# Performance work log

Measured on AMD Instinct MI355X. Metric: run time of the kernel, lower is better.

Reference implementation:

```python
import jax, jax.numpy as jnp
import numpy as np

N = 100000        # nodes
E = 3200000       # random edges (avg degree 32); self-loops added in reference
IN, HID, HEADS, OUT = 10, 32, 2, 4
NEG_SLOPE = 0.2   # PyG GATConv default leaky_relu slope


def setup_inputs() -> dict:
    key = jax.random.key(0)
    ks = jax.random.split(key, 16)
    s = 0.1
    return {
        "x": jax.random.normal(ks[0], (N, IN), jnp.float32),
        "edge_index": jax.random.randint(ks[1], (2, E), 0, N),
        "W1": jax.random.normal(ks[2], (IN, HEADS * HID), jnp.float32) * s,
        "a1s": jax.random.normal(ks[3], (HEADS, HID), jnp.float32) * s,
        "a1d": jax.random.normal(ks[4], (HEADS, HID), jnp.float32) * s,
        "b1": jnp.zeros((HEADS * HID,), jnp.float32),
        "W2": jax.random.normal(ks[5], (HEADS * HID, HEADS * HID), jnp.float32) * s,
        "a2s": jax.random.normal(ks[6], (HEADS, HID), jnp.float32) * s,
        "a2d": jax.random.normal(ks[7], (HEADS, HID), jnp.float32) * s,
        "b2": jnp.zeros((HEADS * HID,), jnp.float32),
        "W3": jax.random.normal(ks[8], (HEADS * HID, OUT), jnp.float32) * s,
        "a3s": jax.random.normal(ks[9], (1, OUT), jnp.float32) * s,
        "a3d": jax.random.normal(ks[10], (1, OUT), jnp.float32) * s,
        "b3": jnp.zeros((OUT,), jnp.float32),
    }


def gat_layer(x, src, dst, W, a_src, a_dst, b, concat):
    """One PyG-style GATConv (shared src/dst linear, self-loops already in src/dst)."""
    heads, oc = a_src.shape
    h = (x @ W).reshape(-1, heads, oc)                    # [N, H, C]
    asc = jnp.einsum('nhc,hc->nh', h, a_src)              # [N, H]
    adc = jnp.einsum('nhc,hc->nh', h, a_dst)              # [N, H]
    e = jax.nn.leaky_relu(asc[src] + adc[dst], NEG_SLOPE) # [Etot, H]
    m = jax.ops.segment_max(e, dst, num_segments=N)       # segment softmax over dst
    ex = jnp.exp(e - m[dst])
    z = jax.ops.segment_sum(ex, dst, num_segments=N)
    alpha = ex / z[dst]                                   # [Etot, H]
    out = jax.ops.segment_sum(h[src] * alpha[:, :, None], dst, num_segments=N)
    out = out.reshape(-1, heads * oc) if concat else out.mean(axis=1)
    return out + b


def reference(x, edge_index, W1, a1s, a1d, b1, W2, a2s, a2d, b2, W3, a3s, a3d, b3):
    loops = jnp.arange(N)
    src = jnp.concatenate([edge_index[0], loops])
    dst = jnp.concatenate([edge_index[1], loops])
    h = jax.nn.relu(gat_layer(x, src, dst, W1, a1s, a1d, b1, True))
    h = jax.nn.relu(gat_layer(h, src, dst, W2, a2s, a2d, b2, True))
    h = gat_layer(h, src, dst, W3, a3s, a3d, b3, False)
    return jax.nn.sigmoid(h) * 100.0
```

## Files before the change

kernel.cpp:

```cpp
#include <hip/hip_runtime.h>
#include <hip/hip_bf16.h>
#include <math.h>

#define NEG_SLOPE 0.2f
#define PSHIFT 8
#define PSIZE 256
#define NPARTS_MAX 392
#define B1 768
#define CELL_CAP 32
#define PCAP 10240
#define LCSR_CAP 10240
#define CHUNK 64

typedef int vint2 __attribute__((ext_vector_type(2)));
typedef int vint4 __attribute__((ext_vector_type(4)));
typedef short bf16x8 __attribute__((ext_vector_type(8)));
typedef float floatx4 __attribute__((ext_vector_type(4)));

__device__ __forceinline__ float lrelu(float v) { return fmaxf(v, NEG_SLOPE * v); }

__device__ __forceinline__ unsigned short f2bf(float f) {
    unsigned int b = __float_as_uint(f);
    b += 0x7fffu + ((b >> 16) & 1u);
    return (unsigned short)(b >> 16);
}
__device__ __forceinline__ float bf2f(unsigned short u) {
    return __uint_as_float((unsigned int)u << 16);
}

__global__ void k_part(const int* __restrict__ src, const int* __restrict__ dst, int E,
                       int* __restrict__ pairs, int* __restrict__ ptot, int nparts) {
    __shared__ int stage[NPARTS_MAX * CELL_CAP];
    __shared__ int lcnt[NPARTS_MAX];
    int tid = threadIdx.x, blk = blockIdx.x;
    for (int i = tid; i < nparts; i += 256) lcnt[i] = 0;
    __syncthreads();
    int per = ((E + B1 * 4 - 1) / (B1 * 4)) * 4;
    int s = blk * per, e = min(E, s + per);
    bool al = ((E & 3) == 0);
    for (int i0 = s + tid * 4; i0 < e; i0 += 1024) {
        int dv[4], sv[4], nv;
        if (al && i0 + 4 <= e) {
            vint4 d4 = __builtin_nontemporal_load((const vint4*)(dst + i0));
            vint4 s4 = __builtin_nontemporal_load((const vint4*)(src + i0));
            dv[0] = d4.x; dv[1] = d4.y; dv[2] = d4.z; dv[3] = d4.w;
            sv[0] = s4.x; sv[1] = s4.y; sv[2] = s4.z; sv[3] = s4.w;
            nv = 4;
        } else {
            nv = min(4, e - i0);
            for (int k = 0; k < nv; ++k) {
                dv[k] = __builtin_nontemporal_load(dst + i0 + k);
                sv[k] = __builtin_nontemporal_load(src + i0 + k);
            }
        }
        for (int k = 0; k < nv; ++k) {
            int p = dv[k] >> PSHIFT;
            int pos = atomicAdd(&lcnt[p], 1);
            if (pos < CELL_CAP)
                stage[p * CELL_CAP + pos] = (sv[k] << PSHIFT) | (dv[k] & (PSIZE - 1));
        }
    }
    __syncthreads();
    for (int p = tid; p < nparts; p += 256) {
        int tgt = min(lcnt[p], CELL_CAP);
        if (tgt == 0) continue;
        int base = atomicAdd(&ptot[p], tgt);
        if (base + tgt > PCAP) tgt = max(0, PCAP - base);
        int* gp = pairs + (size_t)p * PCAP + base;
        const int* sp = &stage[p * CELL_CAP];
        for (int j = 0; j < tgt; ++j) gp[j] = sp[j];
    }
}

__global__ void k_pscan(const int* __restrict__ ptot, int* __restrict__ pbase,
                        int* __restrict__ row, int nparts, int N) {
    __shared__ int sh[512];
    int tid = threadIdx.x;
    int v = (tid < nparts) ? min(ptot[tid], PCAP) : 0;
    sh[tid] = v;
    __syncthreads();
    for (int off = 1; off < 512; off <<= 1) {
        int t = (tid >= off) ? sh[tid - off] : 0;
        __syncthreads();
        sh[tid] += t;
        __syncthreads();
    }
    if (tid < nparts) pbase[tid] = sh[tid] - v;
    if (tid == nparts - 1) row[N] = sh[tid];
}

__global__ void k_scat2(const int* __restrict__ pairs, const int* __restrict__ ptot,
                        const int* __restrict__ pbase, int* __restrict__ row,
                        int* __restrict__ csr, int N) {
    __shared__ int lcsr[LCSR_CAP];
    __shared__ int lhist[PSIZE], lcur[PSIZE];
    int part = blockIdx.x;
    int lo = part << PSHIFT;
    int npart = min(PSIZE, N - lo);
    int tid = threadIdx.x;
    int cnt = min(ptot[part], PCAP);
    const int* seg = pairs + (size_t)part * PCAP;
    for (int i = tid; i < PSIZE; i += 1024) lhist[i] = 0;
    __syncthreads();
    for (int i = tid; i < cnt; i += 1024)
        atomicAdd(&lhist[__builtin_nontemporal_load(&seg[i]) & (PSIZE - 1)], 1);
    __syncthreads();
    if (tid < PSIZE) lcur[tid] = lhist[tid];
    __syncthreads();
    for (int off = 1; off < PSIZE; off <<= 1) {
        int t = 0;
        if (tid < PSIZE && tid >= off) t = lcur[tid - off];
        __syncthreads();
        if (tid < PSIZE) lcur[tid] += t;
        __syncthreads();
    }
    int pb = pbase[part];
    if (tid < npart) row[lo + tid] = pb + lcur[tid] - lhist[tid];
    if (tid < PSIZE) lcur[tid] -= lhist[tid];
    __syncthreads();
    for (int i = tid; i < cnt; i += 1024) {
        int v = __builtin_nontemporal_load(&seg[i]);
        int pos = atomicAdd(&lcur[v & (PSIZE - 1)], 1);
        if (pos < LCSR_CAP) lcsr[pos] = (unsigned)v >> PSHIFT;
    }
    __syncthreads();
    for (int i = tid; i < cnt; i += 1024)
        csr[pb + i] = lcsr[i];
}

__global__ void k_lin1(const float* __restrict__ x, const float* __restrict__ W,
                       const float* __restrict__ as_, const float* __restrict__ ad_,
                       unsigned short* __restrict__ hb, float* __restrict__ asc,
                       float* __restrict__ adc, int N) {
    __shared__ float sW[10 * 64];
    int tid = threadIdx.x;
    for (int i = tid; i < 640; i += 256) sW[i] = W[i];
    __syncthreads();
    int wid = tid >> 6, lane = tid & 63;
    int n = blockIdx.x * 4 + wid;
    if (n >= N) return;
    float acc = 0.f;
#pragma unroll
    for (int k = 0; k < 10; ++k) acc += x[n * 10 + k] * sW[k * 64 + lane];
    hb[(size_t)n * 64 + lane] = f2bf(acc);
    int head = lane >> 5, cc = lane & 31;
    float rs = acc * as_[lane];
    float rd = acc * ad_[lane];
#pragma unroll
    for (int m = 16; m >= 1; m >>= 1) {
        rs += __shfl_xor(rs, m, 64);
        rd += __shfl_xor(rd, m, 64);
    }
    if (cc == 0) { asc[n * 2 + head] = rs; adc[n * 2 + head] = rd; }
}

__global__ void k_lin2(const float* __restrict__ yin, const float* __restrict__ W,
                       const float* __restrict__ as_, const float* __restrict__ ad_,
                       unsigned short* __restrict__ hb, float* __restrict__ asc,
                       float* __restrict__ adc, int N) {
    __shared__ unsigned short sW[64 * 64];
    int tid = threadIdx.x;
    for (int i = tid; i < 4096; i += 256) sW[i] = f2bf(W[i]);
    __syncthreads();
    int wid = tid >> 6, lane = tid & 63;
    int quad = lane >> 4, col = lane & 15;
    bf16x8 bfr[4][2];
#pragma unroll
    for (int blk = 0; blk < 4; ++blk)
#pragma unroll
        for (int kh = 0; kh < 2; ++kh)
#pragma unroll
            for (int j = 0; j < 8; ++j)
                bfr[blk][kh][j] = (short)sW[(kh * 32 + quad * 8 + j) * 64 + blk * 16 + col];
    float asv[4], adv[4];
#pragma unroll
    for (int blk = 0; blk < 4; ++blk) {
        asv[blk] = as_[blk * 16 + col];
        adv[blk] = ad_[blk * 16 + col];
    }
    int tile = blockIdx.x * 4 + wid;
    int nb = tile * 16;
    if (nb >= N) return;
    int mrow = nb + col; if (mrow >= N) mrow = N - 1;
    const float* yr = yin + (size_t)mrow * 64;
    bf16x8 afr[2];
#pragma unroll
    for (int kh = 0; kh < 2; ++kh) {
        const float4* p = (const float4*)(yr + kh * 32 + quad * 8);
        float4 u0 = p[0], u1 = p[1];
        afr[kh][0] = (short)f2bf(u0.x); afr[kh][1] = (short)f2bf(u0.y);
        afr[kh][2] = (short)f2bf(u0.z); afr[kh][3] = (short)f2bf(u0.w);
        afr[kh][4] = (short)f2bf(u1.x); afr[kh][5] = (short)f2bf(u1.y);
        afr[kh][6] = (short)f2bf(u1.z); afr[kh][7] = (short)f2bf(u1.w);
    }
    floatx4 acc[4];
#pragma unroll
    for (int blk = 0; blk < 4; ++blk) {
        acc[blk][0] = 0.f; acc[blk][1] = 0.f; acc[blk][2] = 0.f; acc[blk][3] = 0.f;
        acc[blk] = __builtin_amdgcn_mfma_f32_16x16x32_bf16(afr[0], bfr[blk][0], acc[blk], 0, 0, 0);
        acc[blk] = __builtin_amdgcn_mfma_f32_16x16x32_bf16(afr[1], bfr[blk][1], acc[blk], 0, 0, 0);
    }
#pragma unroll
    for (int r = 0; r < 4; ++r) {
        int m = nb + quad * 4 + r;
        if (m < N) {
#pragma unroll
            for (int blk = 0; blk < 4; ++blk)
                hb[(size_t)m * 64 + blk * 16 + col] = f2bf(acc[blk][r]);
        }
    }
    float s0[4], s1[4], d0[4], d1[4];
#pragma unroll
    for (int r = 0; r < 4; ++r) {
        s0[r] = acc[0][r] * asv[0] + acc[1][r] * asv[1];
        s1[r] = acc[2][r] * asv[2] + acc[3][r] * asv[3];
        d0[r] = acc[0][r] * adv[0] + acc[1][r] * adv[1];
        d1[r] = acc[2][r] * adv[2] + acc[3][r] * adv[3];
    }
#pragma unroll
    for (int mask = 8; mask >= 1; mask >>= 1) {
#pragma unroll
        for (int r = 0; r < 4; ++r) {
            s0[r] += __shfl_xor(s0[r], mask, 64);
            s1[r] += __shfl_xor(s1[r], mask, 64);
            d0[r] += __shfl_xor(d0[r], mask, 64);
            d1[r] += __shfl_xor(d1[r], mask, 64);
        }
    }
    if (col < 4) {
        int m = nb + quad * 4 + col;
        if (m < N) {
            float vs0 = col == 0 ? s0[0] : col == 1 ? s0[1] : col == 2 ? s0[2] : s0[3];
            float vs1 = col == 0 ? s1[0] : col == 1 ? s1[1] : col == 2 ? s1[2] : s1[3];
            float vd0 = col == 0 ? d0[0] : col == 1 ? d0[1] : col == 2 ? d0[2] : d0[3];
            float vd1 = col == 0 ? d1[0] : col == 1 ? d1[1] : col == 2 ? d1[2] : d1[3];
            asc[m * 2 + 0] = vs0; asc[m * 2 + 1] = vs1;
            adc[m * 2 + 0] = vd0; adc[m * 2 + 1] = vd1;
        }
    }
}

__global__ void k_agg(const unsigned short* __restrict__ hb, const float* __restrict__ asc,
                      const float* __restrict__ adc, const int* __restrict__ row,
                      const int* __restrict__ csr_src, const float* __restrict__ bias,
                      float* __restrict__ yout, int N, int do_relu) {
    __shared__ vint2 tbl[4][2 * CHUNK];
    int tid = threadIdx.x;
    int wid = tid >> 6, lane = tid & 63;
    int n = blockIdx.x * 4 + wid;
    if (n >= N) return;
    int s = row[n], e = row[n + 1];
    int head = lane >> 5, sub = lane & 31;
    int cho = lane & 7;
    int hq = (lane >> 2) & 1;
    int jo = lane >> 3;
    int cho16 = cho << 4;
    float2 ad = ((const float2*)adc)[n];
    float adch = head ? ad.y : ad.x;
    float2 asf = ((const float2*)asc)[n];
    float p_self_h = __expf(lrelu((head ? asf.y : asf.x) + adch));
    float zl = (sub == 0) ? p_self_h : 0.f;
    float a0 = 0.f, a1 = 0.f, a2 = 0.f, a3 = 0.f;
    float a4 = 0.f, a5 = 0.f, a6 = 0.f, a7 = 0.f;
    const char* hbB = (const char*)hb;
    vint2* mytbl = tbl[wid];
    int tb = hq << 6;
    int wbase = head << 6;
    for (int base = s; base < e; base += CHUNK) {
        int cnt = e - base; if (cnt > CHUNK) cnt = CHUNK;
#pragma unroll
        for (int h2 = 0; h2 < 2; ++h2) {
            int idx = base + sub + h2 * 32;
            int srcv = 0;
            float p_l = 0.f;
            if (idx < e) {
                srcv = csr_src[idx];
                p_l = __expf(lrelu(asc[(size_t)srcv * 2 + head] + adch));
            }
            zl += p_l;
            vint2 ent; ent.x = srcv << 7; ent.y = __float_as_int(p_l);
            mytbl[wbase | (sub + h2 * 32)] = ent;
        }
        __builtin_amdgcn_wave_barrier();
#pragma unroll 4
        for (int j = jo; j < cnt; j += 8) {
            vint2 t = mytbl[tb | j];
            vint4 pk = *(const vint4*)(hbB + (unsigned)(t.x | cho16));
            float p = __int_as_float(t.y);
            unsigned int w0 = (unsigned int)pk.x, w1 = (unsigned int)pk.y;
            unsigned int w2 = (unsigned int)pk.z, w3 = (unsigned int)pk.w;
            a0 += p * __uint_as_float(w0 << 16);
            a1 += p * __uint_as_float(w0 & 0xffff0000u);
            a2 += p * __uint_as_float(w1 << 16);
            a3 += p * __uint_as_float(w1 & 0xffff0000u);
            a4 += p * __uint_as_float(w2 << 16);
            a5 += p * __uint_as_float(w2 & 0xffff0000u);
            a6 += p * __uint_as_float(w3 << 16);
            a7 += p * __uint_as_float(w3 & 0xffff0000u);
        }
        __builtin_amdgcn_wave_barrier();
    }
#pragma unroll
    for (int msk = 8; msk <= 32; msk <<= 1) {
        a0 += __shfl_xor(a0, msk, 64); a1 += __shfl_xor(a1, msk, 64);
        a2 += __shfl_xor(a2, msk, 64); a3 += __shfl_xor(a3, msk, 64);
        a4 += __shfl_xor(a4, msk, 64); a5 += __shfl_xor(a5, msk, 64);
        a6 += __shfl_xor(a6, msk, 64); a7 += __shfl_xor(a7, msk, 64);
    }
#pragma unroll
    for (int msk = 16; msk >= 1; msk >>= 1) zl += __shfl_xor(zl, msk, 64);
    float zo = __shfl_xor(zl, 32, 64);
    float zneed = (hq == head) ? zl : zo;
    float adcm = hq ? ad.y : ad.x;
    float p_self_my = __expf(lrelu((hq ? asf.y : asf.x) + adcm));
    vint4 pks = *(const vint4*)(hbB + (((unsigned)n << 7) | (unsigned)cho16));
    {
        unsigned int w0 = (unsigned int)pks.x, w1 = (unsigned int)pks.y;
        unsigned int w2 = (unsigned int)pks.z, w3 = (unsigned int)pks.w;
        a0 += p_self_my * __uint_as_float(w0 << 16);
        a1 += p_self_my * __uint_as_float(w0 & 0xffff0000u);
        a2 += p_self_my * __uint_as_float(w1 << 16);
        a3 += p_self_my * __uint_as_float(w1 & 0xffff0000u);
        a4 += p_self_my * __uint_as_float(w2 << 16);
        a5 += p_self_my * __uint_as_float(w2 & 0xffff0000u);
        a6 += p_self_my * __uint_as_float(w3 << 16);
        a7 += p_self_my * __uint_as_float(w3 & 0xffff0000u);
    }
    float inv = 1.f / zneed;
    float4 bv0 = ((const float4*)bias)[cho * 2];
    float4 bv1 = ((const float4*)bias)[cho * 2 + 1];
    float y0 = a0 * inv + bv0.x;
    float y1 = a1 * inv + bv0.y;
    float y2 = a2 * inv + bv0.z;
    float y3 = a3 * inv + bv0.w;
    float y4 = a4 * inv + bv1.x;
    float y5 = a5 * inv + bv1.y;
    float y6 = a6 * inv + bv1.z;
    float y7 = a7 * inv + bv1.w;
    if (do_relu) {
        y0 = fmaxf(y0, 0.f); y1 = fmaxf(y1, 0.f);
        y2 = fmaxf(y2, 0.f); y3 = fmaxf(y3, 0.f);
        y4 = fmaxf(y4, 0.f); y5 = fmaxf(y5, 0.f);
        y6 = fmaxf(y6, 0.f); y7 = fmaxf(y7, 0.f);
    }
    if (jo == 0) {
        float4 o0; o0.x = y0; o0.y = y1; o0.z = y2; o0.w = y3;
        float4 o1; o1.x = y4; o1.y = y5; o1.z = y6; o1.w = y7;
        ((float4*)yout)[(size_t)n * 16 + cho * 2] = o0;
        ((float4*)yout)[(size_t)n * 16 + cho * 2 + 1] = o1;
    }
}

__global__ void k_lin3(const float* __restrict__ yin, const float* __restrict__ W3,
                       const float* __restrict__ a3s, const float* __restrict__ a3d,
                       float4* __restrict__ rec, int N) {
    __shared__ float sW[256];
    int tid = threadIdx.x;
    sW[tid] = W3[tid];
    __syncthreads();
    int t = blockIdx.x * 256 + tid;
    int n = t >> 2, c = t & 3;
    if (n >= N) return;
    float acc = 0.f;
#pragma unroll
    for (int k = 0; k < 64; ++k) acc += yin[(size_t)n * 64 + k] * sW[k * 4 + c];
    float rs = acc * a3s[c], rd = acc * a3d[c];
    rs += __shfl_xor(rs, 1, 64); rs += __shfl_xor(rs, 2, 64);
    rd += __shfl_xor(rd, 1, 64); rd += __shfl_xor(rd, 2, 64);
    float a_1 = __shfl_xor(acc, 1, 64);
    float a_2 = __shfl_xor(acc, 2, 64);
    float a_3 = __shfl_xor(acc, 3, 64);
    if (c == 0) {
        unsigned int lo = (unsigned int)f2bf(acc) | ((unsigned int)f2bf(a_1) << 16);
        unsigned int hi = (unsigned int)f2bf(a_2) | ((unsigned int)f2bf(a_3) << 16);
        float4 r;
        r.x = __uint_as_float(lo); r.y = __uint_as_float(hi);
        r.z = rs; r.w = rd;
        rec[n] = r;
    }
}

__global__ void k_agg3(const float4* __restrict__ rec, const int* __restrict__ row,
                       const int* __restrict__ csr_src, const float* __restrict__ b3,
                       float* __restrict__ out, int N) {
    int tid = threadIdx.x;
    int half = tid >> 5, lane = tid & 31;
    int n = blockIdx.x * 8 + half;
    if (n >= N) return;
    int s = row[n], e = row[n + 1];
    float4 rn = rec[n];
    float adcn = rn.w;
    float n0 = 0.f, n1 = 0.f, n2 = 0.f, n3 = 0.f, den = 0.f;
    if (lane == 0) {
        float p = __expf(lrelu(rn.z + adcn));
        unsigned int lo = __float_as_uint(rn.x), hi = __float_as_uint(rn.y);
        n0 = p * __uint_as_float(lo << 16);
        n1 = p * __uint_as_float(lo & 0xffff0000u);
        n2 = p * __uint_as_float(hi << 16);
        n3 = p * __uint_as_float(hi & 0xffff0000u);
        den = p;
    }
    for (int idx = s + lane; idx < e; idx += 32) {
        int src = csr_src[idx];
        float4 r = rec[src];
        float p = __expf(lrelu(r.z + adcn));
        unsigned int lo = __float_as_uint(r.x), hi = __float_as_uint(r.y);
        n0 += p * __uint_as_float(lo << 16);
        n1 += p * __uint_as_float(lo & 0xffff0000u);
        n2 += p * __uint_as_float(hi << 16);
        n3 += p * __uint_as_float(hi & 0xffff0000u);
        den += p;
    }
#pragma unroll
    for (int msk = 16; msk >= 1; msk >>= 1) {
        n0 += __shfl_xor(n0, msk, 64);
        n1 += __shfl_xor(n1, msk, 64);
        n2 += __shfl_xor(n2, msk, 64);
        n3 += __shfl_xor(n3, msk, 64);
        den += __shfl_xor(den, msk, 64);
    }
    if (lane < 4) {
        float num = lane == 0 ? n0 : lane == 1 ? n1 : lane == 2 ? n2 : n3;
        float v = num / den + b3[lane];
        out[n * 4 + lane] = 100.f / (1.f + __expf(-v));
    }
}

extern "C" void kernel_launch(void* const* d_in, const int* in_sizes, int n_in,
                              void* d_out, int out_size, void* d_ws, size_t ws_size,
                              hipStream_t stream) {
    const float* x   = (const float*)d_in[0];
    const int*   ei  = (const int*)d_in[1];
    const float* W1  = (const float*)d_in[2];
    const float* a1s = (const float*)d_in[3];
    const float* a1d = (const float*)d_in[4];
    const float* b1  = (const float*)d_in[5];
    const float* W2  = (const float*)d_in[6];
    const float* a2s = (const float*)d_in[7];
    const float* a2d = (const float*)d_in[8];
    const float* b2  = (const float*)d_in[9];
    const float* W3  = (const float*)d_in[10];
    const float* a3s = (const float*)d_in[11];
    const float* a3d = (const float*)d_in[12];
    const float* b3  = (const float*)d_in[13];
    float* out = (float*)d_out;

    const int N = in_sizes[0] / 10;
    const int E = in_sizes[1] / 2;
    const int* esrc = ei;
    const int* edst = ei + E;
    const int nparts = (N + PSIZE - 1) >> PSHIFT;

    char* ws = (char*)d_ws;
    size_t off = 0;
    auto alloc = [&](size_t bytes) {
        void* p = ws + off;
        off = (off + bytes + 255) & ~(size_t)255;
        return p;
    };
    int*   row   = (int*)alloc((size_t)(N + 1) * sizeof(int));
    int*   ptot  = (int*)alloc(NPARTS_MAX * sizeof(int));
    int*   pbase = (int*)alloc(NPARTS_MAX * sizeof(int));
    int*   csr   = (int*)alloc((size_t)E * sizeof(int));
    unsigned short* hb = (unsigned short*)alloc((size_t)N * 64 * sizeof(unsigned short));
    float* y     = (float*)alloc((size_t)N * 64 * sizeof(float));
    float4* rec  = (float4*)alloc((size_t)N * sizeof(float4));
    float* asc   = (float*)alloc((size_t)N * 2 * sizeof(float));
    float* adc   = (float*)alloc((size_t)N * 2 * sizeof(float));
    int* pairs = (int*)hb;

    (void)hipMemsetAsync(ptot, 0, NPARTS_MAX * sizeof(int), stream);

    const int nw = (N + 3) / 4;
    const int tiles = (N + 15) / 16;

    k_part<<<B1, 256, 0, stream>>>(esrc, edst, E, pairs, ptot, nparts);
    k_pscan<<<1, 512, 0, stream>>>(ptot, pbase, row, nparts, N);
    k_scat2<<<nparts, 1024, 0, stream>>>(pairs, ptot, pbase, row, csr, N);

    k_lin1<<<nw, 256, 0, stream>>>(x, W1, a1s, a1d, hb, asc, adc, N);
    k_agg<<<nw, 256, 0, stream>>>(hb, asc, adc, row, csr, b1, y, N, 1);
    k_lin2<<<(tiles + 3) / 4, 256, 0, stream>>>(y, W2, a2s, a2d, hb, asc, adc, N);
    k_agg<<<nw, 256, 0, stream>>>(hb, asc, adc, row, csr, b2, y, N, 1);
    k_lin3<<<(N * 4 + 255) / 256, 256, 0, stream>>>(y, W3, a3s, a3d, rec, N);
    k_agg3<<<(N + 7) / 8, 256, 0, stream>>>(rec, row, csr, b3, out, N);
}
```

Baseline: 355.4 us.

## Replace LDS edge table with wave shuffles and add nontemporal streaming accesses

The aggregation kernel no longer stages each 64-edge chunk's source offsets and attention weights in LDS. Each lane now loads one edge, computes the weights for both heads from a single float2 read of asc, and the inner loop broadcasts values with shuffles, removing the LDS table and wave barriers. The layer-3 projection is restructured so each lane reads 16 contiguous floats as vectors and computes partial dots for all four outputs before a shuffle reduction. Nontemporal loads and stores are added for streamed arrays such as csr_src, yin, yout and out. The cost is three shuffles per edge iteration in place of one LDS read, and a risk that nontemporal hints hurt if the data would have been reused from cache.

```diff
diff --git a/kernel.cpp b/kernel.cpp
--- a/kernel.cpp
+++ b/kernel.cpp
@@ -10,7 +10,6 @@
 #define CELL_CAP 32
 #define PCAP 10240
 #define LCSR_CAP 10240
-#define CHUNK 64
 
 typedef int vint2 __attribute__((ext_vector_type(2)));
 typedef int vint4 __attribute__((ext_vector_type(4)));
@@ -186,12 +185,13 @@
     bf16x8 afr[2];
 #pragma unroll
     for (int kh = 0; kh < 2; ++kh) {
-        const float4* p = (const float4*)(yr + kh * 32 + quad * 8);
-        float4 u0 = p[0], u1 = p[1];
-        afr[kh][0] = (short)f2bf(u0.x); afr[kh][1] = (short)f2bf(u0.y);
-        afr[kh][2] = (short)f2bf(u0.z); afr[kh][3] = (short)f2bf(u0.w);
-        afr[kh][4] = (short)f2bf(u1.x); afr[kh][5] = (short)f2bf(u1.y);
-        afr[kh][6] = (short)f2bf(u1.z); afr[kh][7] = (short)f2bf(u1.w);
+        const floatx4* p = (const floatx4*)(yr + kh * 32 + quad * 8);
+        floatx4 u0 = __builtin_nontemporal_load(p);
+        floatx4 u1 = __builtin_nontemporal_load(p + 1);
+        afr[kh][0] = (short)f2bf(u0[0]); afr[kh][1] = (short)f2bf(u0[1]);
+        afr[kh][2] = (short)f2bf(u0[2]); afr[kh][3] = (short)f2bf(u0[3]);
+        afr[kh][4] = (short)f2bf(u1[0]); afr[kh][5] = (short)f2bf(u1[1]);
+        afr[kh][6] = (short)f2bf(u1[2]); afr[kh][7] = (short)f2bf(u1[3]);
     }
     floatx4 acc[4];
 #pragma unroll
@@ -244,49 +244,39 @@
                       const float* __restrict__ adc, const int* __restrict__ row,
                       const int* __restrict__ csr_src, const float* __restrict__ bias,
                       float* __restrict__ yout, int N, int do_relu) {
-    __shared__ vint2 tbl[4][2 * CHUNK];
     int tid = threadIdx.x;
     int wid = tid >> 6, lane = tid & 63;
     int n = blockIdx.x * 4 + wid;
     if (n >= N) return;
     int s = row[n], e = row[n + 1];
-    int head = lane >> 5, sub = lane & 31;
     int cho = lane & 7;
     int hq = (lane >> 2) & 1;
     int jo = lane >> 3;
     int cho16 = cho << 4;
     float2 ad = ((const float2*)adc)[n];
-    float adch = head ? ad.y : ad.x;
     float2 asf = ((const float2*)asc)[n];
-    float p_self_h = __expf(lrelu((head ? asf.y : asf.x) + adch));
-    float zl = (sub == 0) ? p_self_h : 0.f;
     float a0 = 0.f, a1 = 0.f, a2 = 0.f, a3 = 0.f;
     float a4 = 0.f, a5 = 0.f, a6 = 0.f, a7 = 0.f;
+    float z0 = 0.f, z1 = 0.f;
     const char* hbB = (const char*)hb;
-    vint2* mytbl = tbl[wid];
-    int tb = hq << 6;
-    int wbase = head << 6;
-    for (int base = s; base < e; base += CHUNK) {
-        int cnt = e - base; if (cnt > CHUNK) cnt = CHUNK;
-#pragma unroll
-        for (int h2 = 0; h2 < 2; ++h2) {
-            int idx = base + sub + h2 * 32;
-            int srcv = 0;
-            float p_l = 0.f;
-            if (idx < e) {
-                srcv = csr_src[idx];
-                p_l = __expf(lrelu(asc[(size_t)srcv * 2 + head] + adch));
-            }
-            zl += p_l;
-            vint2 ent; ent.x = srcv << 7; ent.y = __float_as_int(p_l);
-            mytbl[wbase | (sub + h2 * 32)] = ent;
-        }
-        __builtin_amdgcn_wave_barrier();
+    for (int base = s; base < e; base += 64) {
+        int cnt = e - base; if (cnt > 64) cnt = 64;
+        int sv7 = 0; float p0 = 0.f, p1 = 0.f;
+        if (lane < cnt) {
+            int srcv = __builtin_nontemporal_load(csr_src + base + lane);
+            float2 av = ((const float2*)asc)[srcv];
+            p0 = __expf(lrelu(av.x + ad.x));
+            p1 = __expf(lrelu(av.y + ad.y));
+            sv7 = srcv << 7;
+        }
+        z0 += p0; z1 += p1;
 #pragma unroll 4
         for (int j = jo; j < cnt; j += 8) {
-            vint2 t = mytbl[tb | j];
-            vint4 pk = *(const vint4*)(hbB + (unsigned)(t.x | cho16));
-            float p = __int_as_float(t.y);
+            int a = __shfl(sv7, j, 64);
+            float q0 = __shfl(p0, j, 64);
+            float q1 = __shfl(p1, j, 64);
+            float p = hq ? q1 : q0;
+            vint4 pk = *(const vint4*)(hbB + (unsigned)(a | cho16));
             unsigned int w0 = (unsigned int)pk.x, w1 = (unsigned int)pk.y;
             unsigned int w2 = (unsigned int)pk.z, w3 = (unsigned int)pk.w;
             a0 += p * __uint_as_float(w0 << 16);
@@ -298,7 +288,6 @@
             a6 += p * __uint_as_float(w3 << 16);
             a7 += p * __uint_as_float(w3 & 0xffff0000u);
         }
-        __builtin_amdgcn_wave_barrier();
     }
 #pragma unroll
     for (int msk = 8; msk <= 32; msk <<= 1) {
@@ -308,11 +297,15 @@
         a6 += __shfl_xor(a6, msk, 64); a7 += __shfl_xor(a7, msk, 64);
     }
 #pragma unroll
-    for (int msk = 16; msk >= 1; msk >>= 1) zl += __shfl_xor(zl, msk, 64);
-    float zo = __shfl_xor(zl, 32, 64);
-    float zneed = (hq == head) ? zl : zo;
-    float adcm = hq ? ad.y : ad.x;
-    float p_self_my = __expf(lrelu((hq ? asf.y : asf.x) + adcm));
+    for (int msk = 1; msk <= 32; msk <<= 1) {
+        z0 += __shfl_xor(z0, msk, 64);
+        z1 += __shfl_xor(z1, msk, 64);
+    }
+    float ps0 = __expf(lrelu(asf.x + ad.x));
+    float ps1 = __expf(lrelu(asf.y + ad.y));
+    z0 += ps0; z1 += ps1;
+    float p_self_my = hq ? ps1 : ps0;
+    float zneed = hq ? z1 : z0;
     vint4 pks = *(const vint4*)(hbB + (((unsigned)n << 7) | (unsigned)cho16));
     {
         unsigned int w0 = (unsigned int)pks.x, w1 = (unsigned int)pks.y;
@@ -344,10 +337,11 @@
         y6 = fmaxf(y6, 0.f); y7 = fmaxf(y7, 0.f);
     }
     if (jo == 0) {
-        float4 o0; o0.x = y0; o0.y = y1; o0.z = y2; o0.w = y3;
-        float4 o1; o1.x = y4; o1.y = y5; o1.z = y6; o1.w = y7;
-        ((float4*)yout)[(size_t)n * 16 + cho * 2] = o0;
-        ((float4*)yout)[(size_t)n * 16 + cho * 2 + 1] = o1;
+        floatx4 o0; o0[0] = y0; o0[1] = y1; o0[2] = y2; o0[3] = y3;
+        floatx4 o1; o1[0] = y4; o1[1] = y5; o1[2] = y6; o1[3] = y7;
+        floatx4* yp = (floatx4*)yout + (size_t)n * 16 + cho * 2;
+        __builtin_nontemporal_store(o0, yp);
+        __builtin_nontemporal_store(o1, yp + 1);
     }
 }
 
@@ -361,18 +355,30 @@
     int t = blockIdx.x * 256 + tid;
     int n = t >> 2, c = t & 3;
     if (n >= N) return;
-    float acc = 0.f;
-#pragma unroll
-    for (int k = 0; k < 64; ++k) acc += yin[(size_t)n * 64 + k] * sW[k * 4 + c];
-    float rs = acc * a3s[c], rd = acc * a3d[c];
-    rs += __shfl_xor(rs, 1, 64); rs += __shfl_xor(rs, 2, 64);
-    rd += __shfl_xor(rd, 1, 64); rd += __shfl_xor(rd, 2, 64);
-    float a_1 = __shfl_xor(acc, 1, 64);
-    float a_2 = __shfl_xor(acc, 2, 64);
-    float a_3 = __shfl_xor(acc, 3, 64);
+    float d0 = 0.f, d1 = 0.f, d2 = 0.f, d3 = 0.f;
+    const floatx4* yr = (const floatx4*)(yin + (size_t)n * 64 + c * 16);
+#pragma unroll
+    for (int k4 = 0; k4 < 4; ++k4) {
+        floatx4 v = __builtin_nontemporal_load(yr + k4);
+        int kb = (c * 16 + k4 * 4) * 4;
+        d0 += v[0] * sW[kb + 0];  d1 += v[0] * sW[kb + 1];
+        d2 += v[0] * sW[kb + 2];  d3 += v[0] * sW[kb + 3];
+        d0 += v[1] * sW[kb + 4];  d1 += v[1] * sW[kb + 5];
+        d2 += v[1] * sW[kb + 6];  d3 += v[1] * sW[kb + 7];
+        d0 += v[2] * sW[kb + 8];  d1 += v[2] * sW[kb + 9];
+        d2 += v[2] * sW[kb + 10]; d3 += v[2] * sW[kb + 11];
+        d0 += v[3] * sW[kb + 12]; d1 += v[3] * sW[kb + 13];
+        d2 += v[3] * sW[kb + 14]; d3 += v[3] * sW[kb + 15];
+    }
+    d0 += __shfl_xor(d0, 1, 64); d1 += __shfl_xor(d1, 1, 64);
+    d2 += __shfl_xor(d2, 1, 64); d3 += __shfl_xor(d3, 1, 64);
+    d0 += __shfl_xor(d0, 2, 64); d1 += __shfl_xor(d1, 2, 64);
+    d2 += __shfl_xor(d2, 2, 64); d3 += __shfl_xor(d3, 2, 64);
     if (c == 0) {
-        unsigned int lo = (unsigned int)f2bf(acc) | ((unsigned int)f2bf(a_1) << 16);
-        unsigned int hi = (unsigned int)f2bf(a_2) | ((unsigned int)f2bf(a_3) << 16);
+        float rs = d0 * a3s[0] + d1 * a3s[1] + d2 * a3s[2] + d3 * a3s[3];
+        float rd = d0 * a3d[0] + d1 * a3d[1] + d2 * a3d[2] + d3 * a3d[3];
+        unsigned int lo = (unsigned int)f2bf(d0) | ((unsigned int)f2bf(d1) << 16);
+        unsigned int hi = (unsigned int)f2bf(d2) | ((unsigned int)f2bf(d3) << 16);
         float4 r;
         r.x = __uint_as_float(lo); r.y = __uint_as_float(hi);
         r.z = rs; r.w = rd;
@@ -401,7 +407,7 @@
         den = p;
     }
     for (int idx = s + lane; idx < e; idx += 32) {
-        int src = csr_src[idx];
+        int src = __builtin_nontemporal_load(csr_src + idx);
         float4 r = rec[src];
         float p = __expf(lrelu(r.z + adcn));
         unsigned int lo = __float_as_uint(r.x), hi = __float_as_uint(r.y);
@@ -422,7 +428,7 @@
     if (lane < 4) {
         float num = lane == 0 ? n0 : lane == 1 ? n1 : lane == 2 ? n2 : n3;
         float v = num / den + b3[lane];
-        out[n * 4 + lane] = 100.f / (1.f + __expf(-v));
+        __builtin_nontemporal_store(100.f / (1.f + __expf(-v)), out + n * 4 + lane);
     }
 }
 
```

After: 363.2 us. 1.02x slower.
